# Kernel tuning notes

Measured on AMD Instinct MI355X. Metric: run time of the kernel, lower is better.

Reference implementation:

```python
import jax, jax.numpy as jnp
import numpy as np

B, L, H = 256, 256, 1024
NUM_HEADS = 16
DIM_PER_HEAD = H // NUM_HEADS  # 64
# faithful to source: scale = (dim_per_head // num_heads) ** -0.5 = (64//16)**-0.5 = 0.5
SCALE = (DIM_PER_HEAD // NUM_HEADS) ** (-0.5)
LN_EPS = 1e-5


def setup_inputs() -> dict:
    key = jax.random.key(0)
    ks = jax.random.split(key, 12)
    s = 1.0 / np.sqrt(H)
    return {
        "key": jax.random.normal(ks[0], (B, L, H), dtype=jnp.float32),
        "value": jax.random.normal(ks[1], (B, L, H), dtype=jnp.float32),
        "query": jax.random.normal(ks[2], (B, 1, H), dtype=jnp.float32),
        "attn_mask": jax.random.randint(ks[3], (B, 1, L), 0, 2).astype(bool),
        "Wq": jax.random.uniform(ks[4], (H, H), jnp.float32, -s, s),
        "bq": jnp.zeros((H,), jnp.float32),
        "Wk": jax.random.uniform(ks[5], (H, H), jnp.float32, -s, s),
        "bk": jnp.zeros((H,), jnp.float32),
        "Wv": jax.random.uniform(ks[6], (H, H), jnp.float32, -s, s),
        "bv": jnp.zeros((H,), jnp.float32),
        "Wf": jax.random.uniform(ks[7], (H, H), jnp.float32, -s, s),
        "bf": jnp.zeros((H,), jnp.float32),
        "gamma": jnp.ones((H,), jnp.float32),
        "beta": jnp.zeros((H,), jnp.float32),
    }


def _split_heads(x):
    # [B, L, H] -> [B, heads, L, d]
    b, l, _ = x.shape
    return x.reshape(b, l, NUM_HEADS, DIM_PER_HEAD).transpose(0, 2, 1, 3)


def reference(key, value, query, attn_mask, Wq, bq, Wk, bk, Wv, bv, Wf, bf, gamma, beta):
    residual = query  # [B, 1, H]
    k = _split_heads(key @ Wk.T + bk)      # [B, h, L, d]
    v = _split_heads(value @ Wv.T + bv)    # [B, h, L, d]
    q = _split_heads(query @ Wq.T + bq)    # [B, h, 1, d]

    scores = jnp.einsum('bhqd,bhkd->bhqk', q, k) * SCALE  # [B, h, 1, L]
    mask = attn_mask[:, None, :, :]                       # [B, 1, 1, L]
    scores = jnp.where(mask, -jnp.inf, scores)
    attention = jax.nn.softmax(scores, axis=-1)           # [B, h, 1, L]

    context = jnp.einsum('bhqk,bhkd->bhqd', attention, v)  # [B, h, 1, d]
    context = context.transpose(0, 2, 1, 3).reshape(query.shape[0], -1, H)  # [B, 1, H]

    out = context @ Wf.T + bf
    x = residual + out
    mu = jnp.mean(x, axis=-1, keepdims=True)
    var = jnp.mean(jnp.square(x - mu), axis=-1, keepdims=True)
    out = (x - mu) * jax.lax.rsqrt(var + LN_EPS) * gamma + beta

    # attention returned as [B*heads, 1, L] like torch bmm layout
    attn_flat = attention.reshape(query.shape[0] * NUM_HEADS, 1, -1)
    return out, attn_flat
```

## Files before the change

kernel.cpp:

```cpp
#include <hip/hip_runtime.h>
#include <math.h>

#define BB 256
#define LL 256
#define HH 1024
#define NH 16
#define DD 64
#define SCALE 0.5f
#define LN_EPS 1e-5f
#define NEG_BIG (-3.402823466e38f)

#define FMA4(accv, vq, s)                \
  accv.x = fmaf(vq.x, s, accv.x);       \
  accv.y = fmaf(vq.y, s, accv.y);       \
  accv.z = fmaf(vq.z, s, accv.z);       \
  accv.w = fmaf(vq.w, s, accv.w);

__device__ __forceinline__ void gl_lds16(const float* gsrc, float* ldst) {
  __builtin_amdgcn_global_load_lds(
      (const __attribute__((address_space(1))) unsigned int*)gsrc,
      (__attribute__((address_space(3))) unsigned int*)ldst, 16, 0, 0);
}

__global__ __launch_bounds__(256) void t_tr(const float* __restrict__ in,
                                            float* __restrict__ out, int inRS,
                                            int outRS, int inPlane,
                                            int outPlane) {
  __shared__ float lds[64][68];
  const float* ip = in + (size_t)blockIdx.z * inPlane;
  float* op = out + (size_t)blockIdx.z * outPlane;
  const int rt = blockIdx.y, ct = blockIdx.x;
  const int lr = threadIdx.x >> 4;
  const int lc = (threadIdx.x & 15) * 4;
#pragma unroll
  for (int p = 0; p < 4; p++) {
    float4 v = *(const float4*)(ip + (size_t)(rt * 64 + p * 16 + lr) * inRS +
                                ct * 64 + lc);
    *(float4*)(&lds[p * 16 + lr][lc]) = v;
  }
  __syncthreads();
#pragma unroll
  for (int p = 0; p < 4; p++) {
    float4 v = make_float4(lds[lc + 0][p * 16 + lr], lds[lc + 1][p * 16 + lr],
                           lds[lc + 2][p * 16 + lr], lds[lc + 3][p * 16 + lr]);
    *(float4*)(op + (size_t)(ct * 64 + p * 16 + lr) * outRS + rt * 64 + lc) = v;
  }
}

__global__ __launch_bounds__(256) void k1_qproj(const float* __restrict__ Wq,
                                                const float* __restrict__ qTT,
                                                const float* __restrict__ bq,
                                                float* __restrict__ qT) {
  __shared__ float smem[10240];
  const int jt = blockIdx.x;
  const int boff = blockIdx.y * 8;
  const int t = threadIdx.x;
  const int g = __builtin_amdgcn_readfirstlane(t >> 6);
  const int ln = t & 63;
  float* kw = smem + g * 2560;
  const float* Wb = Wq + (size_t)(jt * 64) * HH;
  const int srow = ln >> 2, sc = ln & 3;

  float acc[8];
#pragma unroll
  for (int c = 0; c < 8; c++) acc[c] = 0.f;
  float4 pf[4];
#pragma unroll
  for (int p = 0; p < 4; p++)
    pf[p] = *(const float4*)(Wb + (size_t)(p * 16 + srow) * HH + g * 16 + sc * 4);
  int buf = 0;
  for (int T = 0; T < 16; T++) {
    float* kb = kw + buf * 1280;
#pragma unroll
    for (int p = 0; p < 4; p++)
      *(float4*)(kb + ((p * 16 + srow) * 5 + sc) * 4) = pf[p];
    if (T < 15) {
      const int off = (T + 1) * 64 + g * 16 + sc * 4;
#pragma unroll
      for (int p = 0; p < 4; p++)
        pf[p] = *(const float4*)(Wb + (size_t)(p * 16 + srow) * HH + off);
    }
    const int i0 = T * 64 + g * 16;
#pragma unroll
    for (int u = 0; u < 4; u++) {
      float4 kv = *(const float4*)(kb + (ln * 5 + u) * 4);
      const float* q0 = qTT + (size_t)(i0 + u * 4 + 0) * BB + boff;
      const float* q1 = qTT + (size_t)(i0 + u * 4 + 1) * BB + boff;
      const float* q2 = qTT + (size_t)(i0 + u * 4 + 2) * BB + boff;
      const float* q3 = qTT + (size_t)(i0 + u * 4 + 3) * BB + boff;
#pragma unroll
      for (int c = 0; c < 8; c++) {
        acc[c] = fmaf(kv.x, q0[c], acc[c]);
        acc[c] = fmaf(kv.y, q1[c], acc[c]);
        acc[c] = fmaf(kv.z, q2[c], acc[c]);
        acc[c] = fmaf(kv.w, q3[c], acc[c]);
      }
    }
    buf ^= 1;
  }
  __syncthreads();
  float* part = smem;
  *(float4*)(part + g * 768 + ln * 12 + 0) =
      make_float4(acc[0], acc[1], acc[2], acc[3]);
  *(float4*)(part + g * 768 + ln * 12 + 4) =
      make_float4(acc[4], acc[5], acc[6], acc[7]);
  __syncthreads();
  const int j = t & 63, c0 = (t >> 6) * 2;
  float v0 = 0.f, v1 = 0.f;
#pragma unroll
  for (int g2 = 0; g2 < 4; g2++) {
    v0 += part[g2 * 768 + j * 12 + c0];
    v1 += part[g2 * 768 + j * 12 + c0 + 1];
  }
  const int jg = jt * 64 + j;
  const float bias = bq[jg];
  *(float2*)(qT + (size_t)jg * BB + boff + c0) =
      make_float2(v0 + bias, v1 + bias);
}

__global__ __launch_bounds__(256) void k2_qk(const float* __restrict__ qT,
                                             const float* __restrict__ Wk,
                                             float* __restrict__ qkT) {
  const int h = blockIdx.y;
  const int it = blockIdx.x;
  const int il = threadIdx.x & 63;
  const int bs = __builtin_amdgcn_readfirstlane(threadIdx.x >> 6);
  const int i = it * 64 + il;
  const int boff = blockIdx.z * 64 + bs * 16;
  float acc[16];
#pragma unroll
  for (int k = 0; k < 16; k++) acc[k] = 0.f;
#pragma unroll 2
  for (int d = 0; d < DD; d++) {
    float wv = Wk[(size_t)(h * DD + d) * HH + i];
    const float* qrow = qT + (h * DD + d) * BB + boff;
#pragma unroll
    for (int k = 0; k < 16; k++) acc[k] = fmaf(qrow[k], wv, acc[k]);
  }
#pragma unroll
  for (int k = 0; k < 16; k++)
    qkT[(size_t)((boff + k) * NH + h) * HH + i] = SCALE * acc[k];
}

__global__ __launch_bounds__(256) void k2b_relayout(
    const float* __restrict__ qkT, float* __restrict__ qkR) {
  __shared__ float lds[16][268];
  const int b = blockIdx.y, seg = blockIdx.x;
  const int t = threadIdx.x;
  const int row = t >> 4, l16 = t & 15;
  const float* src = qkT + (size_t)b * 16384 + row * HH + seg * 256 + l16 * 16;
#pragma unroll
  for (int p = 0; p < 4; p++)
    *(float4*)(&lds[row][l16 * 16 + p * 4]) = *(const float4*)(src + p * 4);
  __syncthreads();
  const int c = t & 63;
  const int i4g = t >> 6;
  const int h = c >> 2, i3 = c & 3;
  float* dst = qkR + (size_t)b * 16384 + seg * 4096;
#pragma unroll
  for (int jj = 0; jj < 16; jj++) {
    const int i4l = i4g * 16 + jj;
    dst[i4l * 64 + c] = lds[h][i4l * 4 + i3];
  }
}

__global__ __launch_bounds__(256) void k3a_scores(
    const float* __restrict__ key, const int* __restrict__ mask,
    const float* __restrict__ qkR, float* __restrict__ scoresT) {
  __shared__ float kbuf[2][4096];
  __shared__ float qbuf[2][1024];
  const int b = blockIdx.y;
  const int lt = blockIdx.x;
  const int t = threadIdx.x;
  const int g = __builtin_amdgcn_readfirstlane(t >> 6);
  const int ln = t & 63;
  const int m15 = ln & 15;
  const int g4 = ln >> 4;

  const float* keyb = key + ((size_t)(b * LL + lt * 64)) * HH;
  const float* qkb = qkR + (size_t)b * 16384;

  const int srow = t >> 4;
  const int sunit = (t & 15) ^ srow;
  const float* ks0 = keyb + (size_t)(srow + 0) * HH + sunit * 4;
  const float* ks1 = keyb + (size_t)(srow + 16) * HH + sunit * 4;
  const float* ks2 = keyb + (size_t)(srow + 32) * HH + sunit * 4;
  const float* ks3 = keyb + (size_t)(srow + 48) * HH + sunit * 4;
  const float* qs = qkb + t * 4;

  gl_lds16(ks0, &kbuf[0][t * 4 + 0]);
  gl_lds16(ks1, &kbuf[0][t * 4 + 1024]);
  gl_lds16(ks2, &kbuf[0][t * 4 + 2048]);
  gl_lds16(ks3, &kbuf[0][t * 4 + 3072]);
  gl_lds16(qs, &qbuf[0][t * 4]);
  __syncthreads();

  float acc[4][4];
#pragma unroll
  for (int r = 0; r < 4; r++)
#pragma unroll
    for (int h = 0; h < 4; h++) acc[r][h] = 0.f;

  for (int c = 0; c < 16; c++) {
    if (c < 15) {
      const int nb = (c + 1) & 1;
      const int co = (c + 1) * 64;
      gl_lds16(ks0 + co, &kbuf[nb][t * 4 + 0]);
      gl_lds16(ks1 + co, &kbuf[nb][t * 4 + 1024]);
      gl_lds16(ks2 + co, &kbuf[nb][t * 4 + 2048]);
      gl_lds16(ks3 + co, &kbuf[nb][t * 4 + 3072]);
      gl_lds16(qs + (c + 1) * 1024, &qbuf[nb][t * 4]);
    }
    const float* kb = kbuf[c & 1];
    const float* qb = qbuf[c & 1];
#pragma unroll
    for (int iq = 0; iq < 4; iq++) {
      const int U = g4 * 4 + iq;
      const float* qu = qb + U * 64 + g * 16;
      float4 q0 = *(const float4*)(qu + 0);
      float4 q1 = *(const float4*)(qu + 4);
      float4 q2 = *(const float4*)(qu + 8);
      float4 q3 = *(const float4*)(qu + 12);
      const int slot4 = (U ^ m15) * 4;
#pragma unroll
      for (int r = 0; r < 4; r++) {
        float4 kv = *(const float4*)(kb + (m15 + 16 * r) * 64 + slot4);
        acc[r][0] = fmaf(kv.x, q0.x, acc[r][0]);
        acc[r][0] = fmaf(kv.y, q0.y, acc[r][0]);
        acc[r][0] = fmaf(kv.z, q0.z, acc[r][0]);
        acc[r][0] = fmaf(kv.w, q0.w, acc[r][0]);
        acc[r][1] = fmaf(kv.x, q1.x, acc[r][1]);
        acc[r][1] = fmaf(kv.y, q1.y, acc[r][1]);
        acc[r][1] = fmaf(kv.z, q1.z, acc[r][1]);
        acc[r][1] = fmaf(kv.w, q1.w, acc[r][1]);
        acc[r][2] = fmaf(kv.x, q2.x, acc[r][2]);
        acc[r][2] = fmaf(kv.y, q2.y, acc[r][2]);
        acc[r][2] = fmaf(kv.z, q2.z, acc[r][2]);
        acc[r][2] = fmaf(kv.w, q2.w, acc[r][2]);
        acc[r][3] = fmaf(kv.x, q3.x, acc[r][3]);
        acc[r][3] = fmaf(kv.y, q3.y, acc[r][3]);
        acc[r][3] = fmaf(kv.z, q3.z, acc[r][3]);
        acc[r][3] = fmaf(kv.w, q3.w, acc[r][3]);
      }
    }
    __syncthreads();
  }

#pragma unroll
  for (int r = 0; r < 4; r++)
#pragma unroll
    for (int h = 0; h < 4; h++) {
      acc[r][h] += __shfl_xor(acc[r][h], 16);
      acc[r][h] += __shfl_xor(acc[r][h], 32);
    }

  float o0 = acc[0][0], o1 = acc[0][1], o2 = acc[0][2], o3 = acc[0][3];
  if (g4 == 1) { o0 = acc[1][0]; o1 = acc[1][1]; o2 = acc[1][2]; o3 = acc[1][3]; }
  if (g4 == 2) { o0 = acc[2][0]; o1 = acc[2][1]; o2 = acc[2][2]; o3 = acc[2][3]; }
  if (g4 == 3) { o0 = acc[3][0]; o1 = acc[3][1]; o2 = acc[3][2]; o3 = acc[3][3]; }

  const int l = lt * 64 + 16 * g4 + m15;
  const int mk = mask[b * LL + l];
  if (mk) { o0 = NEG_BIG; o1 = NEG_BIG; o2 = NEG_BIG; o3 = NEG_BIG; }
  scoresT[((size_t)(b * NH + g * 4 + 0)) * LL + l] = o0;
  scoresT[((size_t)(b * NH + g * 4 + 1)) * LL + l] = o1;
  scoresT[((size_t)(b * NH + g * 4 + 2)) * LL + l] = o2;
  scoresT[((size_t)(b * NH + g * 4 + 3)) * LL + l] = o3;
}

__global__ __launch_bounds__(256) void k3b_softmax(float* __restrict__ attn) {
  const int r = blockIdx.x * 4 + (threadIdx.x >> 6);
  const int lane = threadIdx.x & 63;
  float* rowp = attn + (size_t)r * LL;
  float4 s = *(const float4*)(rowp + lane * 4);
  float m = fmaxf(fmaxf(s.x, s.y), fmaxf(s.z, s.w));
#pragma unroll
  for (int off = 32; off >= 1; off >>= 1) m = fmaxf(m, __shfl_xor(m, off));
  float ex = __expf(s.x - m), ey = __expf(s.y - m), ez = __expf(s.z - m),
        ew = __expf(s.w - m);
  float e = ex + ey + ez + ew;
#pragma unroll
  for (int off = 32; off >= 1; off >>= 1) e += __shfl_xor(e, off);
  float inv = 1.0f / e;
  *(float4*)(rowp + lane * 4) = make_float4(ex * inv, ey * inv, ez * inv, ew * inv);
}

__global__ __launch_bounds__(256) void k3c_vbar(
    const float* __restrict__ value, const float* __restrict__ attn,
    float* __restrict__ vbar) {
  __shared__ float alds[4096];
  const int b = blockIdx.y;
  const int dt = blockIdx.x;
  const int t = threadIdx.x;
  const int g = __builtin_amdgcn_readfirstlane(t >> 6);
  const int ln = t & 63;
  const float* ab = attn + (size_t)b * 4096;
#pragma unroll
  for (int j = 0; j < 4; j++)
    *(float4*)(alds + j * 1024 + t * 4) = *(const float4*)(ab + j * 1024 + t * 4);
  __syncthreads();

  const int d0 = dt * 256 + ln * 4;
  const float* valb = value + (size_t)b * LL * HH + d0;
  const float* aw = alds + g * 4 * 256;

  float4 ac0 = make_float4(0.f, 0.f, 0.f, 0.f);
  float4 ac1 = ac0, ac2 = ac0, ac3 = ac0;

  float4 vf0 = *(const float4*)(valb + (size_t)0 * HH);
  float4 vf1 = *(const float4*)(valb + (size_t)1 * HH);
  float4 vf2 = *(const float4*)(valb + (size_t)2 * HH);
  float4 vf3 = *(const float4*)(valb + (size_t)3 * HH);

#pragma unroll 4
  for (int lq = 0; lq < 64; lq++) {
    float4 v0 = vf0, v1 = vf1, v2 = vf2, v3 = vf3;
    if (lq < 63) {
      vf0 = *(const float4*)(valb + (size_t)((lq + 1) * 4 + 0) * HH);
      vf1 = *(const float4*)(valb + (size_t)((lq + 1) * 4 + 1) * HH);
      vf2 = *(const float4*)(valb + (size_t)((lq + 1) * 4 + 2) * HH);
      vf3 = *(const float4*)(valb + (size_t)((lq + 1) * 4 + 3) * HH);
    }
    float4 a0 = *(const float4*)(aw + 0 * 256 + lq * 4);
    float4 a1 = *(const float4*)(aw + 1 * 256 + lq * 4);
    float4 a2 = *(const float4*)(aw + 2 * 256 + lq * 4);
    float4 a3 = *(const float4*)(aw + 3 * 256 + lq * 4);
    FMA4(ac0, v0, a0.x); FMA4(ac0, v1, a0.y); FMA4(ac0, v2, a0.z); FMA4(ac0, v3, a0.w);
    FMA4(ac1, v0, a1.x); FMA4(ac1, v1, a1.y); FMA4(ac1, v2, a1.z); FMA4(ac1, v3, a1.w);
    FMA4(ac2, v0, a2.x); FMA4(ac2, v1, a2.y); FMA4(ac2, v2, a2.z); FMA4(ac2, v3, a2.w);
    FMA4(ac3, v0, a3.x); FMA4(ac3, v1, a3.y); FMA4(ac3, v2, a3.z); FMA4(ac3, v3, a3.w);
  }
  float* vb = vbar + ((size_t)(b * NH + g * 4)) * HH + d0;
  *(float4*)(vb + 0 * HH) = ac0;
  *(float4*)(vb + 1 * HH) = ac1;
  *(float4*)(vb + 2 * HH) = ac2;
  *(float4*)(vb + 3 * HH) = ac3;
}

__global__ __launch_bounds__(256) void k4_ctx(const float* __restrict__ Wv,
                                              const float* __restrict__ vbarT,
                                              const float* __restrict__ bv,
                                              float* __restrict__ ctxT) {
  __shared__ float smem[10240];
  const int jt = blockIdx.x;
  const int boff = blockIdx.y * 8;
  const int t = threadIdx.x;
  const int g = __builtin_amdgcn_readfirstlane(t >> 6);
  const int ln = t & 63;
  float* kw = smem + g * 2560;
  const float* Wb = Wv + (size_t)(jt * 64) * HH;
  const float* vt = vbarT + (size_t)jt * HH * BB;
  const int srow = ln >> 2, sc = ln & 3;

  float acc[8];
#pragma unroll
  for (int c = 0; c < 8; c++) acc[c] = 0.f;
  float4 pf[4];
#pragma unroll
  for (int p = 0; p < 4; p++)
    pf[p] = *(const float4*)(Wb + (size_t)(p * 16 + srow) * HH + g * 16 + sc * 4);
  int buf = 0;
  for (int T = 0; T < 16; T++) {
    float* kb = kw + buf * 1280;
#pragma unroll
    for (int p = 0; p < 4; p++)
      *(float4*)(kb + ((p * 16 + srow) * 5 + sc) * 4) = pf[p];
    if (T < 15) {
      const int off = (T + 1) * 64 + g * 16 + sc * 4;
#pragma unroll
      for (int p = 0; p < 4; p++)
        pf[p] = *(const float4*)(Wb + (size_t)(p * 16 + srow) * HH + off);
    }
    const int i0 = T * 64 + g * 16;
#pragma unroll
    for (int u = 0; u < 4; u++) {
      float4 kv = *(const float4*)(kb + (ln * 5 + u) * 4);
      const float* q0 = vt + (size_t)(i0 + u * 4 + 0) * BB + boff;
      const float* q1 = vt + (size_t)(i0 + u * 4 + 1) * BB + boff;
      const float* q2 = vt + (size_t)(i0 + u * 4 + 2) * BB + boff;
      const float* q3 = vt + (size_t)(i0 + u * 4 + 3) * BB + boff;
#pragma unroll
      for (int c = 0; c < 8; c++) {
        acc[c] = fmaf(kv.x, q0[c], acc[c]);
        acc[c] = fmaf(kv.y, q1[c], acc[c]);
        acc[c] = fmaf(kv.z, q2[c], acc[c]);
        acc[c] = fmaf(kv.w, q3[c], acc[c]);
      }
    }
    buf ^= 1;
  }
  __syncthreads();
  float* part = smem;
  *(float4*)(part + g * 768 + ln * 12 + 0) =
      make_float4(acc[0], acc[1], acc[2], acc[3]);
  *(float4*)(part + g * 768 + ln * 12 + 4) =
      make_float4(acc[4], acc[5], acc[6], acc[7]);
  __syncthreads();
  const int j = t & 63, c0 = (t >> 6) * 2;
  float v0 = 0.f, v1 = 0.f;
#pragma unroll
  for (int g2 = 0; g2 < 4; g2++) {
    v0 += part[g2 * 768 + j * 12 + c0];
    v1 += part[g2 * 768 + j * 12 + c0 + 1];
  }
  const int jg = jt * 64 + j;
  const float bias = bv[jg];
  *(float2*)(ctxT + (size_t)jg * BB + boff + c0) =
      make_float2(v0 + bias, v1 + bias);
}

__global__ __launch_bounds__(256) void k5_outproj(
    const float* __restrict__ Wf, const float* __restrict__ ctxT,
    const float* __restrict__ bf, const float* __restrict__ query,
    float* __restrict__ xws) {
  __shared__ float smem[10240];
  const int jt = blockIdx.x;
  const int boff = blockIdx.y * 8;
  const int t = threadIdx.x;
  const int g = __builtin_amdgcn_readfirstlane(t >> 6);
  const int ln = t & 63;
  float* kw = smem + g * 2560;
  const float* Wb = Wf + (size_t)(jt * 64) * HH;
  const int srow = ln >> 2, sc = ln & 3;

  float acc[8];
#pragma unroll
  for (int c = 0; c < 8; c++) acc[c] = 0.f;
  float4 pf[4];
#pragma unroll
  for (int p = 0; p < 4; p++)
    pf[p] = *(const float4*)(Wb + (size_t)(p * 16 + srow) * HH + g * 16 + sc * 4);
  int buf = 0;
  for (int T = 0; T < 16; T++) {
    float* kb = kw + buf * 1280;
#pragma unroll
    for (int p = 0; p < 4; p++)
      *(float4*)(kb + ((p * 16 + srow) * 5 + sc) * 4) = pf[p];
    if (T < 15) {
      const int off = (T + 1) * 64 + g * 16 + sc * 4;
#pragma unroll
      for (int p = 0; p < 4; p++)
        pf[p] = *(const float4*)(Wb + (size_t)(p * 16 + srow) * HH + off);
    }
    const int i0 = T * 64 + g * 16;
#pragma unroll
    for (int u = 0; u < 4; u++) {
      float4 kv = *(const float4*)(kb + (ln * 5 + u) * 4);
      const float* q0 = ctxT + (size_t)(i0 + u * 4 + 0) * BB + boff;
      const float* q1 = ctxT + (size_t)(i0 + u * 4 + 1) * BB + boff;
      const float* q2 = ctxT + (size_t)(i0 + u * 4 + 2) * BB + boff;
      const float* q3 = ctxT + (size_t)(i0 + u * 4 + 3) * BB + boff;
#pragma unroll
      for (int c = 0; c < 8; c++) {
        acc[c] = fmaf(kv.x, q0[c], acc[c]);
        acc[c] = fmaf(kv.y, q1[c], acc[c]);
        acc[c] = fmaf(kv.z, q2[c], acc[c]);
        acc[c] = fmaf(kv.w, q3[c], acc[c]);
      }
    }
    buf ^= 1;
  }
  __syncthreads();
  float* part = smem;
  *(float4*)(part + g * 768 + ln * 12 + 0) =
      make_float4(acc[0], acc[1], acc[2], acc[3]);
  *(float4*)(part + g * 768 + ln * 12 + 4) =
      make_float4(acc[4], acc[5], acc[6], acc[7]);
  __syncthreads();
  const int j = t & 63, c0 = (t >> 6) * 2;
  float v0 = 0.f, v1 = 0.f;
#pragma unroll
  for (int g2 = 0; g2 < 4; g2++) {
    v0 += part[g2 * 768 + j * 12 + c0];
    v1 += part[g2 * 768 + j * 12 + c0 + 1];
  }
  const int jg = jt * 64 + j;
  const float bias = bf[jg];
  const int b0 = boff + c0;
  xws[(size_t)b0 * HH + jg] = v0 + bias + query[(size_t)b0 * HH + jg];
  xws[(size_t)(b0 + 1) * HH + jg] = v1 + bias + query[(size_t)(b0 + 1) * HH + jg];
}

__global__ __launch_bounds__(256) void k6_ln(const float* __restrict__ xws,
                                             const float* __restrict__ gamma,
                                             const float* __restrict__ beta,
                                             float* __restrict__ out0) {
  __shared__ float rb[8];
  const int b = blockIdx.x, t = threadIdx.x;
  float4 v = *(const float4*)(xws + (size_t)b * HH + 4 * t);
  float s = v.x + v.y + v.z + v.w;
#pragma unroll
  for (int off = 32; off >= 1; off >>= 1) s += __shfl_xor(s, off);
  if ((t & 63) == 0) rb[t >> 6] = s;
  __syncthreads();
  float mu = (rb[0] + rb[1] + rb[2] + rb[3]) * (1.0f / HH);
  float dx = v.x - mu, dy = v.y - mu, dz = v.z - mu, dw = v.w - mu;
  float q = dx * dx + dy * dy + dz * dz + dw * dw;
#pragma unroll
  for (int off = 32; off >= 1; off >>= 1) q += __shfl_xor(q, off);
  if ((t & 63) == 0) rb[4 + (t >> 6)] = q;
  __syncthreads();
  float var = (rb[4] + rb[5] + rb[6] + rb[7]) * (1.0f / HH);
  float rs = rsqrtf(var + LN_EPS);
  float4 gm = *(const float4*)(gamma + 4 * t);
  float4 bt = *(const float4*)(beta + 4 * t);
  float4 o;
  o.x = dx * rs * gm.x + bt.x;
  o.y = dy * rs * gm.y + bt.y;
  o.z = dz * rs * gm.z + bt.z;
  o.w = dw * rs * gm.w + bt.w;
  *(float4*)(out0 + (size_t)b * HH + 4 * t) = o;
}

extern "C" void kernel_launch(void* const* d_in, const int* in_sizes, int n_in,
                              void* d_out, int out_size, void* d_ws,
                              size_t ws_size, hipStream_t stream) {
  (void)in_sizes; (void)n_in; (void)out_size; (void)ws_size;
  const float* key = (const float*)d_in[0];
  const float* value = (const float*)d_in[1];
  const float* query = (const float*)d_in[2];
  const int* mask = (const int*)d_in[3];
  const float* Wq = (const float*)d_in[4];
  const float* bq = (const float*)d_in[5];
  const float* Wk = (const float*)d_in[6];
  const float* Wv = (const float*)d_in[8];
  const float* bv = (const float*)d_in[9];
  const float* Wf = (const float*)d_in[10];
  const float* bf = (const float*)d_in[11];
  const float* gamma = (const float*)d_in[12];
  const float* beta = (const float*)d_in[13];

  float* out0 = (float*)d_out;
  float* attnOut = out0 + BB * HH;

  char* ws = (char*)d_ws;
  float* qT = (float*)(ws);
  float* qTT = (float*)(ws + (1 << 20));
  float* qkT = (float*)(ws + (2 << 20));
  float* qkR = (float*)(ws + (18 << 20));
  float* vbar = (float*)(ws + (2 << 20));
  float* vbarT = (float*)(ws + (34 << 20));
  float* ctxT = (float*)(ws);
  float* xws = (float*)(ws + (1 << 20));

  t_tr<<<dim3(16, 4, 1), 256, 0, stream>>>(query, qTT, HH, BB, 0, 0);
  k1_qproj<<<dim3(16, 32), 256, 0, stream>>>(Wq, qTT, bq, qT);
  k2_qk<<<dim3(16, 16, 4), 256, 0, stream>>>(qT, Wk, qkT);
  k2b_relayout<<<dim3(4, 256), 256, 0, stream>>>(qkT, qkR);
  k3a_scores<<<dim3(4, 256), 256, 0, stream>>>(key, mask, qkR, attnOut);
  k3b_softmax<<<dim3(1024), 256, 0, stream>>>(attnOut);
  k3c_vbar<<<dim3(4, 256), 256, 0, stream>>>(value, attnOut, vbar);
  t_tr<<<dim3(16, 4, 16), 256, 0, stream>>>(vbar, vbarT, NH * HH, BB, HH,
                                            HH * BB);
  k4_ctx<<<dim3(16, 32), 256, 0, stream>>>(Wv, vbarT, bv, ctxT);
  k5_outproj<<<dim3(16, 32), 256, 0, stream>>>(Wf, ctxT, bf, query, xws);
  k6_ln<<<dim3(256), 256, 0, stream>>>(xws, gamma, beta, out0);
}
```

Baseline: 381.1 us.

## Drop qk relayout kernel and retile scores kernel to 16 key rows per block

Removes the k2b_relayout pass and has the scores kernel read qkT directly, with each block now handling 16 key rows instead of 64, which quadruples the grid. Each thread computes partial dot products over a 4-wide chunk and reduces across 16 lanes with shuffles, then writes a single score. This removes one kernel launch and the qkR round trip through memory. In exchange, each block re-reads the full 64KB qk tile for only 16 key rows, so qk global traffic roughly quadruples, and more shuffle reduction work is added.

```diff
diff --git a/kernel.cpp b/kernel.cpp
--- a/kernel.cpp
+++ b/kernel.cpp
@@ -142,57 +142,27 @@
     qkT[(size_t)((boff + k) * NH + h) * HH + i] = SCALE * acc[k];
 }
 
-__global__ __launch_bounds__(256) void k2b_relayout(
-    const float* __restrict__ qkT, float* __restrict__ qkR) {
-  __shared__ float lds[16][268];
-  const int b = blockIdx.y, seg = blockIdx.x;
-  const int t = threadIdx.x;
-  const int row = t >> 4, l16 = t & 15;
-  const float* src = qkT + (size_t)b * 16384 + row * HH + seg * 256 + l16 * 16;
-#pragma unroll
-  for (int p = 0; p < 4; p++)
-    *(float4*)(&lds[row][l16 * 16 + p * 4]) = *(const float4*)(src + p * 4);
-  __syncthreads();
-  const int c = t & 63;
-  const int i4g = t >> 6;
-  const int h = c >> 2, i3 = c & 3;
-  float* dst = qkR + (size_t)b * 16384 + seg * 4096;
-#pragma unroll
-  for (int jj = 0; jj < 16; jj++) {
-    const int i4l = i4g * 16 + jj;
-    dst[i4l * 64 + c] = lds[h][i4l * 4 + i3];
-  }
-}
-
 __global__ __launch_bounds__(256) void k3a_scores(
     const float* __restrict__ key, const int* __restrict__ mask,
-    const float* __restrict__ qkR, float* __restrict__ scoresT) {
-  __shared__ float kbuf[2][4096];
+    const float* __restrict__ qkT, float* __restrict__ scoresT) {
+  __shared__ float kbuf[2][1024];
   __shared__ float qbuf[2][1024];
   const int b = blockIdx.y;
   const int lt = blockIdx.x;
   const int t = threadIdx.x;
   const int g = __builtin_amdgcn_readfirstlane(t >> 6);
   const int ln = t & 63;
-  const int m15 = ln & 15;
-  const int g4 = ln >> 4;
-
-  const float* keyb = key + ((size_t)(b * LL + lt * 64)) * HH;
-  const float* qkb = qkR + (size_t)b * 16384;
-
-  const int srow = t >> 4;
-  const int sunit = (t & 15) ^ srow;
-  const float* ks0 = keyb + (size_t)(srow + 0) * HH + sunit * 4;
-  const float* ks1 = keyb + (size_t)(srow + 16) * HH + sunit * 4;
-  const float* ks2 = keyb + (size_t)(srow + 32) * HH + sunit * 4;
-  const float* ks3 = keyb + (size_t)(srow + 48) * HH + sunit * 4;
-  const float* qs = qkb + t * 4;
-
-  gl_lds16(ks0, &kbuf[0][t * 4 + 0]);
-  gl_lds16(ks1, &kbuf[0][t * 4 + 1024]);
-  gl_lds16(ks2, &kbuf[0][t * 4 + 2048]);
-  gl_lds16(ks3, &kbuf[0][t * 4 + 3072]);
-  gl_lds16(qs, &qbuf[0][t * 4]);
+  const int sg = ln & 15;
+  const int rq = ln >> 4;
+
+  const float* keyb = key + ((size_t)(b * LL + lt * 16)) * HH;
+  const float* qkb = qkT + (size_t)b * 16384;
+
+  const float* ksrc = keyb + (size_t)(t >> 4) * HH + (t & 15) * 4;
+  const float* qsrc = qkb + (size_t)(t >> 4) * HH + (t & 15) * 4;
+
+  gl_lds16(ksrc, &kbuf[0][t * 4]);
+  gl_lds16(qsrc, &qbuf[0][t * 4]);
   __syncthreads();
 
   float acc[4][4];
@@ -204,44 +174,34 @@
   for (int c = 0; c < 16; c++) {
     if (c < 15) {
       const int nb = (c + 1) & 1;
-      const int co = (c + 1) * 64;
-      gl_lds16(ks0 + co, &kbuf[nb][t * 4 + 0]);
-      gl_lds16(ks1 + co, &kbuf[nb][t * 4 + 1024]);
-      gl_lds16(ks2 + co, &kbuf[nb][t * 4 + 2048]);
-      gl_lds16(ks3 + co, &kbuf[nb][t * 4 + 3072]);
-      gl_lds16(qs + (c + 1) * 1024, &qbuf[nb][t * 4]);
+      gl_lds16(ksrc + (c + 1) * 64, &kbuf[nb][t * 4]);
+      gl_lds16(qsrc + (c + 1) * 64, &qbuf[nb][t * 4]);
     }
     const float* kb = kbuf[c & 1];
     const float* qb = qbuf[c & 1];
-#pragma unroll
-    for (int iq = 0; iq < 4; iq++) {
-      const int U = g4 * 4 + iq;
-      const float* qu = qb + U * 64 + g * 16;
-      float4 q0 = *(const float4*)(qu + 0);
-      float4 q1 = *(const float4*)(qu + 4);
-      float4 q2 = *(const float4*)(qu + 8);
-      float4 q3 = *(const float4*)(qu + 12);
-      const int slot4 = (U ^ m15) * 4;
-#pragma unroll
-      for (int r = 0; r < 4; r++) {
-        float4 kv = *(const float4*)(kb + (m15 + 16 * r) * 64 + slot4);
-        acc[r][0] = fmaf(kv.x, q0.x, acc[r][0]);
-        acc[r][0] = fmaf(kv.y, q0.y, acc[r][0]);
-        acc[r][0] = fmaf(kv.z, q0.z, acc[r][0]);
-        acc[r][0] = fmaf(kv.w, q0.w, acc[r][0]);
-        acc[r][1] = fmaf(kv.x, q1.x, acc[r][1]);
-        acc[r][1] = fmaf(kv.y, q1.y, acc[r][1]);
-        acc[r][1] = fmaf(kv.z, q1.z, acc[r][1]);
-        acc[r][1] = fmaf(kv.w, q1.w, acc[r][1]);
-        acc[r][2] = fmaf(kv.x, q2.x, acc[r][2]);
-        acc[r][2] = fmaf(kv.y, q2.y, acc[r][2]);
-        acc[r][2] = fmaf(kv.z, q2.z, acc[r][2]);
-        acc[r][2] = fmaf(kv.w, q2.w, acc[r][2]);
-        acc[r][3] = fmaf(kv.x, q3.x, acc[r][3]);
-        acc[r][3] = fmaf(kv.y, q3.y, acc[r][3]);
-        acc[r][3] = fmaf(kv.z, q3.z, acc[r][3]);
-        acc[r][3] = fmaf(kv.w, q3.w, acc[r][3]);
-      }
+    float4 q0 = *(const float4*)(qb + (g * 4 + 0) * 64 + sg * 4);
+    float4 q1 = *(const float4*)(qb + (g * 4 + 1) * 64 + sg * 4);
+    float4 q2 = *(const float4*)(qb + (g * 4 + 2) * 64 + sg * 4);
+    float4 q3 = *(const float4*)(qb + (g * 4 + 3) * 64 + sg * 4);
+#pragma unroll
+    for (int r = 0; r < 4; r++) {
+      float4 kv = *(const float4*)(kb + rq * 64 + r * 256 + sg * 4);
+      acc[r][0] = fmaf(kv.x, q0.x, acc[r][0]);
+      acc[r][0] = fmaf(kv.y, q0.y, acc[r][0]);
+      acc[r][0] = fmaf(kv.z, q0.z, acc[r][0]);
+      acc[r][0] = fmaf(kv.w, q0.w, acc[r][0]);
+      acc[r][1] = fmaf(kv.x, q1.x, acc[r][1]);
+      acc[r][1] = fmaf(kv.y, q1.y, acc[r][1]);
+      acc[r][1] = fmaf(kv.z, q1.z, acc[r][1]);
+      acc[r][1] = fmaf(kv.w, q1.w, acc[r][1]);
+      acc[r][2] = fmaf(kv.x, q2.x, acc[r][2]);
+      acc[r][2] = fmaf(kv.y, q2.y, acc[r][2]);
+      acc[r][2] = fmaf(kv.z, q2.z, acc[r][2]);
+      acc[r][2] = fmaf(kv.w, q2.w, acc[r][2]);
+      acc[r][3] = fmaf(kv.x, q3.x, acc[r][3]);
+      acc[r][3] = fmaf(kv.y, q3.y, acc[r][3]);
+      acc[r][3] = fmaf(kv.z, q3.z, acc[r][3]);
+      acc[r][3] = fmaf(kv.w, q3.w, acc[r][3]);
     }
     __syncthreads();
   }
@@ -250,22 +210,34 @@
   for (int r = 0; r < 4; r++)
 #pragma unroll
     for (int h = 0; h < 4; h++) {
-      acc[r][h] += __shfl_xor(acc[r][h], 16);
-      acc[r][h] += __shfl_xor(acc[r][h], 32);
-    }
-
-  float o0 = acc[0][0], o1 = acc[0][1], o2 = acc[0][2], o3 = acc[0][3];
-  if (g4 == 1) { o0 = acc[1][0]; o1 = acc[1][1]; o2 = acc[1][2]; o3 = acc[1][3]; }
-  if (g4 == 2) { o0 = acc[2][0]; o1 = acc[2][1]; o2 = acc[2][2]; o3 = acc[2][3]; }
-  if (g4 == 3) { o0 = acc[3][0]; o1 = acc[3][1]; o2 = acc[3][2]; o3 = acc[3][3]; }
-
-  const int l = lt * 64 + 16 * g4 + m15;
+      acc[r][h] += __shfl_xor(acc[r][h], 1);
+      acc[r][h] += __shfl_xor(acc[r][h], 2);
+      acc[r][h] += __shfl_xor(acc[r][h], 4);
+      acc[r][h] += __shfl_xor(acc[r][h], 8);
+    }
+
+  float o = acc[0][0];
+  if (sg == 1) o = acc[0][1];
+  if (sg == 2) o = acc[0][2];
+  if (sg == 3) o = acc[0][3];
+  if (sg == 4) o = acc[1][0];
+  if (sg == 5) o = acc[1][1];
+  if (sg == 6) o = acc[1][2];
+  if (sg == 7) o = acc[1][3];
+  if (sg == 8) o = acc[2][0];
+  if (sg == 9) o = acc[2][1];
+  if (sg == 10) o = acc[2][2];
+  if (sg == 11) o = acc[2][3];
+  if (sg == 12) o = acc[3][0];
+  if (sg == 13) o = acc[3][1];
+  if (sg == 14) o = acc[3][2];
+  if (sg == 15) o = acc[3][3];
+
+  const int l = lt * 16 + rq + 4 * (sg >> 2);
+  const int h = g * 4 + (sg & 3);
   const int mk = mask[b * LL + l];
-  if (mk) { o0 = NEG_BIG; o1 = NEG_BIG; o2 = NEG_BIG; o3 = NEG_BIG; }
-  scoresT[((size_t)(b * NH + g * 4 + 0)) * LL + l] = o0;
-  scoresT[((size_t)(b * NH + g * 4 + 1)) * LL + l] = o1;
-  scoresT[((size_t)(b * NH + g * 4 + 2)) * LL + l] = o2;
-  scoresT[((size_t)(b * NH + g * 4 + 3)) * LL + l] = o3;
+  if (mk) o = NEG_BIG;
+  scoresT[((size_t)(b * NH + h)) * LL + l] = o;
 }
 
 __global__ __launch_bounds__(256) void k3b_softmax(float* __restrict__ attn) {
@@ -537,8 +509,7 @@
   float* qT = (float*)(ws);
   float* qTT = (float*)(ws + (1 << 20));
   float* qkT = (float*)(ws + (2 << 20));
-  float* qkR = (float*)(ws + (18 << 20));
-  float* vbar = (float*)(ws + (2 << 20));
+  float* vbar = (float*)(ws + (18 << 20));
   float* vbarT = (float*)(ws + (34 << 20));
   float* ctxT = (float*)(ws);
   float* xws = (float*)(ws + (1 << 20));
@@ -546,8 +517,7 @@
   t_tr<<<dim3(16, 4, 1), 256, 0, stream>>>(query, qTT, HH, BB, 0, 0);
   k1_qproj<<<dim3(16, 32), 256, 0, stream>>>(Wq, qTT, bq, qT);
   k2_qk<<<dim3(16, 16, 4), 256, 0, stream>>>(qT, Wk, qkT);
-  k2b_relayout<<<dim3(4, 256), 256, 0, stream>>>(qkT, qkR);
-  k3a_scores<<<dim3(4, 256), 256, 0, stream>>>(key, mask, qkR, attnOut);
+  k3a_scores<<<dim3(16, 256), 256, 0, stream>>>(key, mask, qkT, attnOut);
   k3b_softmax<<<dim3(1024), 256, 0, stream>>>(attnOut);
   k3c_vbar<<<dim3(4, 256), 256, 0, stream>>>(value, attnOut, vbar);
   t_tr<<<dim3(16, 4, 16), 256, 0, stream>>>(vbar, vbarT, NH * HH, BB, HH,
```

New measurement: 430.8 us. 13.1% more time.
